# Performance work log

Hardware: AMD Instinct MI355X
Metric: run time of the kernel (lower is better)

## Reference

```python
import jax, jax.numpy as jnp
import numpy as np

NEG_SLOPE = 0.2  # leaky_relu_negative_slope


def setup_inputs() -> dict:
    key = jax.random.key(0)
    k = jax.random.split(key, 6)
    N = 1024          # n_nodes == nei_nodes (forced by the asserts in forward)
    IN = 256          # in_features
    OUT = 256         # out_features (nei_embedding feature dim, since linear_r = Linear(out_features, ...))
    H, F = 4, 64      # n_heads, n_hidden = out_features // n_heads
    h = jax.random.normal(k[0], (N, IN), dtype=jnp.float32)
    nei_embedding = jax.random.normal(k[1], (N, OUT), dtype=jnp.float32)
    adj_mat = jax.random.randint(k[2], (N, N), 0, 2).astype(jnp.float32)
    scale = 0.05
    w_l = jax.random.normal(k[3], (IN, H * F), dtype=jnp.float32) * scale   # linear_l.weight.T
    w_r = jax.random.normal(k[4], (OUT, H * F), dtype=jnp.float32) * scale  # linear_r.weight.T
    attn_w = jax.random.normal(k[5], (F,), dtype=jnp.float32) * scale       # attn.weight (1, F) -> (F,)
    return {"h": h, "nei_embedding": nei_embedding, "adj_mat": adj_mat,
            "w_l": w_l, "w_r": w_r, "attn_w": attn_w, "use_elu": 1}


def reference(h, nei_embedding, adj_mat, w_l, w_r, attn_w, use_elu):
    N = h.shape[0]
    M = nei_embedding.shape[0]
    F = attn_w.shape[0]
    H = w_l.shape[1] // F
    g_l = (h @ w_l).reshape(N, H, F)              # (N, H, F)
    g_r = (nei_embedding @ w_r).reshape(M, H, F)  # (M, H, F)
    # Torch does repeat/repeat_interleave then view(n, m, H, F); with the
    # assert-enforced n == m this is exactly g_sum[i, j] = g_l[j] + g_r[i].
    g_sum = g_r[:, None, :, :] + g_l[None, :, :, :]          # (N, N, H, F)
    e = jnp.einsum("nmhf,f->nmh", jax.nn.leaky_relu(g_sum, NEG_SLOPE), attn_w)
    adj_t = adj_mat.T[:, :, None]                             # (M, N, 1) -> broadcasts over heads
    e = jnp.where(adj_t == 0, -jnp.inf, e)
    exp_attention = jnp.exp(e)
    weighted = exp_attention * adj_t                          # (N, N, H)
    denom = jnp.sum(weighted, axis=1, keepdims=True)
    a = weighted / denom                                      # masked softmax over neighbors
    # dropout is identity at inference
    attn_res = jnp.einsum("ijh,jhf->ihf", a, g_r)            # (N, H, F)
    if use_elu:
        attn_res = jax.nn.elu(attn_res)
    return attn_res.reshape(N, H * F)  # is_concat=True
```

## Files before the change

kernel.cpp:

```cpp
#include <hip/hip_runtime.h>
#include <math.h>

#define NN 1024
#define KK 256
#define NH 4
#define FD 64
#define HF 256

typedef __attribute__((ext_vector_type(16))) float fx16;

#define OFF_GL   0
#define OFF_GR   (256*1024)
#define OFF_CL   (512*1024)
#define OFF_CR   (512*1024 + 4096)
#define OFF_DENP (512*1024 + 8192)
#define OFF_P    (768*1024)
#define OFF_ACCP (OFF_P + 4*1024*1024)

__global__ __launch_bounds__(256) void gatv2_gemm(
    const float* __restrict__ hmat, const float* __restrict__ nei,
    const float* __restrict__ w_l, const float* __restrict__ w_r,
    const float* __restrict__ aw, float* __restrict__ ws)
{
    __shared__ float sA[16*260];
    const int t   = threadIdx.x;
    const int mb  = blockIdx.x;
    const int hd  = blockIdx.y;
    const int mat = blockIdx.z;
    const float* A = mat ? nei : hmat;
    const float* W = mat ? w_r : w_l;
    float* G  = ws + (mat ? OFF_GR : OFF_GL);
    float* CC = ws + (mat ? OFF_CR : OFF_CL);

    #pragma unroll
    for (int rep = 0; rep < 4; ++rep) {
        const int flat = rep*256 + t;
        const int r = flat >> 6, c = (flat & 63) << 2;
        *(float4*)&sA[r*260 + c] = *(const float4*)&A[(size_t)(mb*16 + r)*KK + c];
    }
    __syncthreads();

    const int m  = t >> 4;
    const int nq = t & 15;
    const int ng = hd*64 + (nq << 2);
    const float* Wp = W + ng;

    float4 acc = make_float4(0.f, 0.f, 0.f, 0.f);
    #pragma unroll 4
    for (int k0 = 0; k0 < KK; k0 += 4) {
        const float4 a4 = *(const float4*)&sA[m*260 + k0];
        const float4 w0 = *(const float4*)(Wp + (size_t)(k0+0)*HF);
        const float4 w1 = *(const float4*)(Wp + (size_t)(k0+1)*HF);
        const float4 w2 = *(const float4*)(Wp + (size_t)(k0+2)*HF);
        const float4 w3 = *(const float4*)(Wp + (size_t)(k0+3)*HF);
        acc.x += a4.x*w0.x; acc.y += a4.x*w0.y; acc.z += a4.x*w0.z; acc.w += a4.x*w0.w;
        acc.x += a4.y*w1.x; acc.y += a4.y*w1.y; acc.z += a4.y*w1.z; acc.w += a4.y*w1.w;
        acc.x += a4.z*w2.x; acc.y += a4.z*w2.y; acc.z += a4.z*w2.z; acc.w += a4.z*w2.w;
        acc.x += a4.w*w3.x; acc.y += a4.w*w3.y; acc.z += a4.w*w3.z; acc.w += a4.w*w3.w;
    }

    *(float4*)&G[(size_t)(mb*16 + m)*HF + ng] = acc;

    {
        const float4 w4 = ((const float4*)aw)[nq];
        float wd = w4.x*acc.x + w4.y*acc.y + w4.z*acc.z + w4.w*acc.w;
        wd += __shfl_xor(wd, 1);
        wd += __shfl_xor(wd, 2);
        wd += __shfl_xor(wd, 4);
        wd += __shfl_xor(wd, 8);
        if (nq == 0) CC[hd*NN + mb*16 + m] = 0.6f*wd;
    }
}

#define EBLK(RV, QB)                                                \
    { _Pragma("unroll") for (int q = 0; q < 4; ++q) {               \
        const float4 wq = w[(QB)+q]; const float4 gq = gri[(QB)+q]; \
        e0 += wq.x * fabsf(RV[q*4+0] + gq.x);                       \
        e1 += wq.y * fabsf(RV[q*4+1] + gq.y);                       \
        e2 += wq.z * fabsf(RV[q*4+2] + gq.z);                       \
        e3 += wq.w * fabsf(RV[q*4+3] + gq.w); } }

__global__ __launch_bounds__(256, 3) void gatv2_e(
    const float* __restrict__ wsro, const float* __restrict__ adj,
    const float* __restrict__ aw, float* __restrict__ P,
    float* __restrict__ denP)
{
    const float* g_l = wsro + OFF_GL;
    const float* g_r = wsro + OFF_GR;
    const float* cl  = wsro + OFF_CL;
    const float* cr  = wsro + OFF_CR;
    const int t  = threadIdx.x;
    const int jc = blockIdx.x;
    const int ib = blockIdx.y;
    const int hh = blockIdx.z;
    const int i  = ib*256 + t;

    float4 w[16], gri[16];
    {
        const float4* awp = (const float4*)aw;
        const float4* gp  = (const float4*)(g_r + (size_t)i*HF + hh*FD);
        #pragma unroll
        for (int q = 0; q < 16; ++q) { w[q] = awp[q]; gri[q] = gp[q]; }
    }
    const float cri = cr[hh*NN + i];

    float denl = 0.f;
    const int j0 = jc*32;
    for (int jj = 0; jj < 32; ++jj) {
        const int j = j0 + jj;
        const float mask = adj[(size_t)j*NN + i];
        fx16 r0, r1, r2, r3; float clv;
        const float* rowp = g_l + (size_t)j*HF + hh*FD;
        const float* clp  = cl + hh*NN + j;
        asm volatile(
            "s_load_dwordx16 %0, %5, 0x0\n\t"
            "s_load_dwordx16 %1, %5, 0x40\n\t"
            "s_load_dwordx16 %2, %5, 0x80\n\t"
            "s_load_dwordx16 %3, %5, 0xc0\n\t"
            "s_load_dword %4, %6, 0x0\n\t"
            "s_waitcnt lgkmcnt(0)"
            : "=s"(r0), "=s"(r1), "=s"(r2), "=s"(r3), "=s"(clv)
            : "s"(rowp), "s"(clp));
        float e0 = 0.f, e1 = 0.f, e2 = 0.f, e3 = 0.f;
        EBLK(r0, 0) EBLK(r1, 4) EBLK(r2, 8) EBLK(r3, 12)
        const float e  = cri + clv + 0.4f*((e0+e1)+(e2+e3));
        const float pw = (mask != 0.f) ? __expf(e) : 0.f;
        denl += pw;
        P[((size_t)hh*NN + j)*NN + i] = pw;
    }
    denP[(size_t)jc*(NN*NH) + hh*NN + i] = denl;
}

__global__ __launch_bounds__(256) void gatv2_pv(
    const float* __restrict__ wsro, float* __restrict__ accP, int JC2)
{
    __shared__ float sT[128*65];
    const float* g_r = wsro + OFF_GR;
    const float* P   = wsro + OFF_P;
    const int t  = threadIdx.x;
    const int jc = blockIdx.x;
    const int ib = blockIdx.y;
    const int hh = blockIdx.z;
    const int wv = t >> 6, l = t & 63;
    const int i1 = ib*128 + l;
    const int f0 = hh*FD + wv*16;
    const int JPB = NN / JC2;

    float4 a1[4] = {}, a2[4] = {};
    const int j0 = jc*JPB;
    #pragma unroll 2
    for (int jj = 0; jj < JPB; ++jj) {
        const int j = j0 + jj;
        const float* rp = g_r + (size_t)j*HF + f0;
        const float4 r0 = ((const float4*)rp)[0];
        const float4 r1 = ((const float4*)rp)[1];
        const float4 r2 = ((const float4*)rp)[2];
        const float4 r3 = ((const float4*)rp)[3];
        const size_t pbase = ((size_t)hh*NN + j)*NN + i1;
        const float p1 = P[pbase];
        const float p2 = P[pbase + 64];
        a1[0].x += p1*r0.x; a1[0].y += p1*r0.y; a1[0].z += p1*r0.z; a1[0].w += p1*r0.w;
        a1[1].x += p1*r1.x; a1[1].y += p1*r1.y; a1[1].z += p1*r1.z; a1[1].w += p1*r1.w;
        a1[2].x += p1*r2.x; a1[2].y += p1*r2.y; a1[2].z += p1*r2.z; a1[2].w += p1*r2.w;
        a1[3].x += p1*r3.x; a1[3].y += p1*r3.y; a1[3].z += p1*r3.z; a1[3].w += p1*r3.w;
        a2[0].x += p2*r0.x; a2[0].y += p2*r0.y; a2[0].z += p2*r0.z; a2[0].w += p2*r0.w;
        a2[1].x += p2*r1.x; a2[1].y += p2*r1.y; a2[1].z += p2*r1.z; a2[1].w += p2*r1.w;
        a2[2].x += p2*r2.x; a2[2].y += p2*r2.y; a2[2].z += p2*r2.z; a2[2].w += p2*r2.w;
        a2[3].x += p2*r3.x; a2[3].y += p2*r3.y; a2[3].z += p2*r3.z; a2[3].w += p2*r3.w;
    }

    #pragma unroll
    for (int c = 0; c < 4; ++c) {
        *(float4*)&sT[(l     )*65 + wv*16 + c*4] = a1[c];
        *(float4*)&sT[(l + 64)*65 + wv*16 + c*4] = a2[c];
    }
    __syncthreads();
    #pragma unroll
    for (int rep = 0; rep < 8; ++rep) {
        const int flat = rep*1024 + t*4;
        const int il = flat >> 6, f = flat & 63;
        const float4 v = *(const float4*)&sT[il*65 + f];
        *(float4*)&accP[(size_t)jc*(NN*HF) + (size_t)(ib*128 + il)*HF + hh*64 + f] = v;
    }
}

__global__ __launch_bounds__(256) void gatv2_fin(
    const float* __restrict__ accP, const float* __restrict__ denP,
    const int* __restrict__ use_elu, float* __restrict__ out, int JC2)
{
    const int idx4 = blockIdx.x*256 + threadIdx.x;
    const int i  = idx4 >> 6;
    const int hh = (idx4 >> 4) & 3;
    float4 s = make_float4(0.f,0.f,0.f,0.f);
    for (int c = 0; c < JC2; ++c) {
        const float4 v = *(const float4*)&accP[(size_t)c*(NN*HF) + (size_t)idx4*4];
        s.x += v.x; s.y += v.y; s.z += v.z; s.w += v.w;
    }
    float d = 0.f;
    for (int c = 0; c < 32; ++c) d += denP[(size_t)c*(NN*NH) + hh*NN + i];
    const float rd = 1.f / d;
    float4 r = make_float4(s.x*rd, s.y*rd, s.z*rd, s.w*rd);
    if (*use_elu != 0) {
        r.x = (r.x > 0.f) ? r.x : expm1f(r.x);
        r.y = (r.y > 0.f) ? r.y : expm1f(r.y);
        r.z = (r.z > 0.f) ? r.z : expm1f(r.z);
        r.w = (r.w > 0.f) ? r.w : expm1f(r.w);
    }
    ((float4*)out)[idx4] = r;
}

extern "C" void kernel_launch(void* const* d_in, const int* in_sizes, int n_in,
                              void* d_out, int out_size, void* d_ws, size_t ws_size,
                              hipStream_t stream)
{
    const float* hmat = (const float*)d_in[0];
    const float* nei  = (const float*)d_in[1];
    const float* adj  = (const float*)d_in[2];
    const float* w_l  = (const float*)d_in[3];
    const float* w_r  = (const float*)d_in[4];
    const float* aw   = (const float*)d_in[5];
    const int*   uel  = (const int*)d_in[6];
    float* out = (float*)d_out;
    float* ws  = (float*)d_ws;

    int JC2 = 16;
    if (((size_t)OFF_ACCP + (size_t)16*NN*HF) * 4 > ws_size) JC2 = 8;

    hipLaunchKernelGGL(gatv2_gemm, dim3(64,4,2), dim3(256), 0, stream,
                       hmat, nei, w_l, w_r, aw, ws);
    hipLaunchKernelGGL(gatv2_e, dim3(32,4,4), dim3(256), 0, stream,
                       ws, adj, aw, ws + OFF_P, ws + OFF_DENP);
    hipLaunchKernelGGL(gatv2_pv, dim3(JC2,8,4), dim3(256), 0, stream,
                       ws, ws + OFF_ACCP, JC2);
    hipLaunchKernelGGL(gatv2_fin, dim3((NN*HF)/1024), dim3(256), 0, stream,
                       ws + OFF_ACCP, ws + OFF_DENP, uel, out, JC2);
}
```

Before: 157.8 us.

## Restructure PV kernel to scalar-load g_r rows with double buffering

The P·V kernel now gives each thread one row i and 32 features, reading the wave-uniform g_r rows through software-pipelined scalar loads (s_load_dwordx16) with double buffering, so g_r traffic moves off the vector memory path. The grid becomes (16,4,8), splitting each head across two 32-feature halves. The workspace fallback to JC2=8 is removed and the split is hard-coded to 16. The e kernel also stages attn_w through shared memory instead of having every thread load it from global memory.

Result: faster. 145.8 us (-7.6%).

```diff
diff --git a/kernel.cpp b/kernel.cpp
--- a/kernel.cpp
+++ b/kernel.cpp
@@ -85,6 +85,7 @@
     const float* __restrict__ aw, float* __restrict__ P,
     float* __restrict__ denP)
 {
+    __shared__ float s_w[64];
     const float* g_l = wsro + OFF_GL;
     const float* g_r = wsro + OFF_GR;
     const float* cl  = wsro + OFF_CL;
@@ -95,12 +96,17 @@
     const int hh = blockIdx.z;
     const int i  = ib*256 + t;
 
+    if (t < 16) ((float4*)s_w)[t] = ((const float4*)aw)[t];
+    __syncthreads();
+
     float4 w[16], gri[16];
     {
-        const float4* awp = (const float4*)aw;
-        const float4* gp  = (const float4*)(g_r + (size_t)i*HF + hh*FD);
+        const float4* gp = (const float4*)(g_r + (size_t)i*HF + hh*FD);
         #pragma unroll
-        for (int q = 0; q < 16; ++q) { w[q] = awp[q]; gri[q] = gp[q]; }
+        for (int q = 0; q < 16; ++q) {
+            w[q]   = ((const float4*)s_w)[q];
+            gri[q] = gp[q];
+        }
     }
     const float cri = cr[hh*NN + i];
 
@@ -131,68 +137,92 @@
     denP[(size_t)jc*(NN*NH) + hh*NN + i] = denl;
 }
 
-__global__ __launch_bounds__(256) void gatv2_pv(
-    const float* __restrict__ wsro, float* __restrict__ accP, int JC2)
-{
-    __shared__ float sT[128*65];
+#define PVFMA(G0, G1, PP)                                           \
+    { _Pragma("unroll") for (int q = 0; q < 4; ++q) {               \
+        acc[q].x   += (PP)*G0[q*4+0]; acc[q].y   += (PP)*G0[q*4+1]; \
+        acc[q].z   += (PP)*G0[q*4+2]; acc[q].w   += (PP)*G0[q*4+3]; \
+        acc[4+q].x += (PP)*G1[q*4+0]; acc[4+q].y += (PP)*G1[q*4+1]; \
+        acc[4+q].z += (PP)*G1[q*4+2]; acc[4+q].w += (PP)*G1[q*4+3]; } }
+
+__global__ __launch_bounds__(256, 3) void gatv2_pv(
+    const float* __restrict__ wsro, float* __restrict__ accP)
+{
+    __shared__ float sT[256*36];
     const float* g_r = wsro + OFF_GR;
     const float* P   = wsro + OFF_P;
     const int t  = threadIdx.x;
     const int jc = blockIdx.x;
     const int ib = blockIdx.y;
-    const int hh = blockIdx.z;
-    const int wv = t >> 6, l = t & 63;
-    const int i1 = ib*128 + l;
-    const int f0 = hh*FD + wv*16;
-    const int JPB = NN / JC2;
-
-    float4 a1[4] = {}, a2[4] = {};
-    const int j0 = jc*JPB;
-    #pragma unroll 2
-    for (int jj = 0; jj < JPB; ++jj) {
+    const int fs = blockIdx.z;
+    const int hh = fs >> 1;
+    const int f0 = hh*64 + (fs & 1)*32;
+    const int i  = ib*256 + t;
+
+    float4 acc[8];
+    #pragma unroll
+    for (int q = 0; q < 8; ++q) acc[q] = make_float4(0.f,0.f,0.f,0.f);
+
+    const int j0 = jc*64;
+    const size_t pb0 = ((size_t)hh*NN)*NN + i;
+
+    fx16 a0, a1, b0, b1;
+    {
+        const float* gp = g_r + (size_t)j0*HF + f0;
+        asm volatile(
+            "s_load_dwordx16 %0, %2, 0x0\n\t"
+            "s_load_dwordx16 %1, %2, 0x40\n\t"
+            "s_waitcnt lgkmcnt(0)"
+            : "=s"(a0), "=s"(a1) : "s"(gp));
+    }
+    float pA = P[pb0 + (size_t)j0*NN];
+
+    for (int jj = 0; jj < 64; jj += 2) {
         const int j = j0 + jj;
-        const float* rp = g_r + (size_t)j*HF + f0;
-        const float4 r0 = ((const float4*)rp)[0];
-        const float4 r1 = ((const float4*)rp)[1];
-        const float4 r2 = ((const float4*)rp)[2];
-        const float4 r3 = ((const float4*)rp)[3];
-        const size_t pbase = ((size_t)hh*NN + j)*NN + i1;
-        const float p1 = P[pbase];
-        const float p2 = P[pbase + 64];
-        a1[0].x += p1*r0.x; a1[0].y += p1*r0.y; a1[0].z += p1*r0.z; a1[0].w += p1*r0.w;
-        a1[1].x += p1*r1.x; a1[1].y += p1*r1.y; a1[1].z += p1*r1.z; a1[1].w += p1*r1.w;
-        a1[2].x += p1*r2.x; a1[2].y += p1*r2.y; a1[2].z += p1*r2.z; a1[2].w += p1*r2.w;
-        a1[3].x += p1*r3.x; a1[3].y += p1*r3.y; a1[3].z += p1*r3.z; a1[3].w += p1*r3.w;
-        a2[0].x += p2*r0.x; a2[0].y += p2*r0.y; a2[0].z += p2*r0.z; a2[0].w += p2*r0.w;
-        a2[1].x += p2*r1.x; a2[1].y += p2*r1.y; a2[1].z += p2*r1.z; a2[1].w += p2*r1.w;
-        a2[2].x += p2*r2.x; a2[2].y += p2*r2.y; a2[2].z += p2*r2.z; a2[2].w += p2*r2.w;
-        a2[3].x += p2*r3.x; a2[3].y += p2*r3.y; a2[3].z += p2*r3.z; a2[3].w += p2*r3.w;
-    }
-
-    #pragma unroll
-    for (int c = 0; c < 4; ++c) {
-        *(float4*)&sT[(l     )*65 + wv*16 + c*4] = a1[c];
-        *(float4*)&sT[(l + 64)*65 + wv*16 + c*4] = a2[c];
-    }
+        {
+            const float* gp = g_r + (size_t)(j+1)*HF + f0;
+            asm volatile(
+                "s_load_dwordx16 %0, %2, 0x0\n\t"
+                "s_load_dwordx16 %1, %2, 0x40"
+                : "=s"(b0), "=s"(b1) : "s"(gp));
+        }
+        const float pB = P[pb0 + (size_t)(j+1)*NN];
+        PVFMA(a0, a1, pA)
+        asm volatile("s_waitcnt lgkmcnt(0)");
+        {
+            const int j2 = (jj + 2 < 64) ? (j + 2) : j0;
+            const float* gp = g_r + (size_t)j2*HF + f0;
+            asm volatile(
+                "s_load_dwordx16 %0, %2, 0x0\n\t"
+                "s_load_dwordx16 %1, %2, 0x40"
+                : "=s"(a0), "=s"(a1) : "s"(gp));
+            pA = P[pb0 + (size_t)j2*NN];
+        }
+        PVFMA(b0, b1, pB)
+        asm volatile("s_waitcnt lgkmcnt(0)");
+    }
+
+    #pragma unroll
+    for (int q = 0; q < 8; ++q)
+        *(float4*)&sT[t*36 + q*4] = acc[q];
     __syncthreads();
     #pragma unroll
     for (int rep = 0; rep < 8; ++rep) {
-        const int flat = rep*1024 + t*4;
-        const int il = flat >> 6, f = flat & 63;
-        const float4 v = *(const float4*)&sT[il*65 + f];
-        *(float4*)&accP[(size_t)jc*(NN*HF) + (size_t)(ib*128 + il)*HF + hh*64 + f] = v;
+        const int idx = rep*256 + t;
+        const int il = idx >> 3, fq = idx & 7;
+        const float4 v = *(const float4*)&sT[il*36 + fq*4];
+        *(float4*)&accP[(size_t)jc*(NN*HF) + (size_t)(ib*256 + il)*HF + f0 + fq*4] = v;
     }
 }
 
 __global__ __launch_bounds__(256) void gatv2_fin(
     const float* __restrict__ accP, const float* __restrict__ denP,
-    const int* __restrict__ use_elu, float* __restrict__ out, int JC2)
+    const int* __restrict__ use_elu, float* __restrict__ out)
 {
     const int idx4 = blockIdx.x*256 + threadIdx.x;
     const int i  = idx4 >> 6;
     const int hh = (idx4 >> 4) & 3;
     float4 s = make_float4(0.f,0.f,0.f,0.f);
-    for (int c = 0; c < JC2; ++c) {
+    for (int c = 0; c < 16; ++c) {
         const float4 v = *(const float4*)&accP[(size_t)c*(NN*HF) + (size_t)idx4*4];
         s.x += v.x; s.y += v.y; s.z += v.z; s.w += v.w;
     }
@@ -223,15 +253,12 @@
     float* out = (float*)d_out;
     float* ws  = (float*)d_ws;
 
-    int JC2 = 16;
-    if (((size_t)OFF_ACCP + (size_t)16*NN*HF) * 4 > ws_size) JC2 = 8;
-
     hipLaunchKernelGGL(gatv2_gemm, dim3(64,4,2), dim3(256), 0, stream,
                        hmat, nei, w_l, w_r, aw, ws);
     hipLaunchKernelGGL(gatv2_e, dim3(32,4,4), dim3(256), 0, stream,
                        ws, adj, aw, ws + OFF_P, ws + OFF_DENP);
-    hipLaunchKernelGGL(gatv2_pv, dim3(JC2,8,4), dim3(256), 0, stream,
-                       ws, ws + OFF_ACCP, JC2);
+    hipLaunchKernelGGL(gatv2_pv, dim3(16,4,8), dim3(256), 0, stream,
+                       ws, ws + OFF_ACCP);
     hipLaunchKernelGGL(gatv2_fin, dim3((NN*HF)/1024), dim3(256), 0, stream,
-                       ws + OFF_ACCP, ws + OFF_DENP, uel, out, JC2);
-}
+                       ws + OFF_ACCP, ws + OFF_DENP, uel, out);
+}
```
